# Optimization experiments

Hardware: AMD Instinct MI355X
Metric: run time of the kernel (lower is better)

The kernel has to match this reference:

```python
import jax, jax.numpy as jnp
import numpy as np

C_POW = 8.0  # RGLRU 'c' constant


def setup_inputs() -> dict:
    key = jax.random.key(0)
    ks = jax.random.split(key, 11)
    B, H, K, NB = 4096, 2048, 4, 4
    Hb = H // NB
    s = 1.0 / np.sqrt(H)
    sb = 1.0 / np.sqrt(Hb)
    return {
        "x": jax.random.normal(ks[0], (B, H), jnp.float32),
        "conv_state": jax.random.normal(ks[1], (B, K - 1, H), jnp.float32),
        "rglru_state": jax.random.normal(ks[2], (B, H), jnp.float32),
        "Wg": jax.random.normal(ks[3], (H, H), jnp.float32) * s,
        "Wr": jax.random.normal(ks[4], (H, H), jnp.float32) * s,
        "Wo": jax.random.normal(ks[5], (H, H), jnp.float32) * s,
        "conv_w": jax.random.normal(ks[6], (K, H), jnp.float32) * 0.5,
        "conv_b": jax.random.normal(ks[7], (H,), jnp.float32) * 0.1,
        "Wi": jax.random.normal(ks[8], (NB, Hb, Hb), jnp.float32) * sb,
        "Wrg": jax.random.normal(ks[9], (NB, Hb, Hb), jnp.float32) * sb,
        # a in (0.5, 0.99): valid base for a**(c*r) and sqrt(1 - a^2)
        "a": jax.random.uniform(ks[10], (H,), jnp.float32) * 0.49 + 0.5,
    }


def _block_linear(x, W):
    # x: [B, H], W: [NB, Hb, Hb] block-diagonal linear (torch convention y = x @ W.T per block)
    B = x.shape[0]
    NB, Hb, _ = W.shape
    xb = x.reshape(B, NB, Hb)
    yb = jnp.einsum("bnh,noh->bno", xb, W)
    return yb.reshape(B, NB * Hb)


def reference(x, conv_state, rglru_state, Wg, Wr, Wo, conv_w, conv_b, Wi, Wrg, a):
    # gate branch
    gate = jax.nn.gelu(x @ Wg.T, approximate=False)
    # recurrent branch projection
    xr = x @ Wr.T
    # depthwise causal conv single step: window = [prev K-1 inputs, current]
    window = jnp.concatenate([conv_state, xr[:, None, :]], axis=1)  # [B, K, H]
    xc = jnp.einsum("bkh,kh->bh", window, conv_w) + conv_b
    new_conv_state = window[:, 1:, :]  # [B, K-1, H]
    # RG-LRU single step
    i_t = jax.nn.sigmoid(_block_linear(xc, Wi))
    r_t = jax.nn.sigmoid(_block_linear(xc, Wrg))
    a_t = jnp.power(a, C_POW * r_t)
    multiplier = jnp.sqrt(1.0 - a_t * a_t)
    new_rglru_state = rglru_state * a_t + multiplier * (i_t * xc)
    # output projection of gated state
    out = (gate * new_rglru_state) @ Wo.T
    return out, new_conv_state, new_rglru_state
```

## Files before the change

### kernel.cpp

```cpp
#include <hip/hip_runtime.h>
#include <math.h>

#define BB 4096
#define HH 2048
#define NBK 4
#define HB 512

typedef short bh8 __attribute__((ext_vector_type(8)));
typedef float f32x4 __attribute__((ext_vector_type(4)));

__device__ __forceinline__ float gelu_exact(float v) {
    return 0.5f * v * (1.0f + erff(v * 0.70710678118654752f));
}

__device__ __forceinline__ void cvt_store(char* hiB, char* loB, int row, int cb,
                                          float4 f0, float4 f1) {
    unsigned u0 = __float_as_uint(f0.x), u1 = __float_as_uint(f0.y),
             u2 = __float_as_uint(f0.z), u3 = __float_as_uint(f0.w),
             u4 = __float_as_uint(f1.x), u5 = __float_as_uint(f1.y),
             u6 = __float_as_uint(f1.z), u7 = __float_as_uint(f1.w);
    uint4 H;
    H.x = (u1 & 0xFFFF0000u) | (u0 >> 16);
    H.y = (u3 & 0xFFFF0000u) | (u2 >> 16);
    H.z = (u5 & 0xFFFF0000u) | (u4 >> 16);
    H.w = (u7 & 0xFFFF0000u) | (u6 >> 16);
    float l0 = f0.x - __uint_as_float(u0 & 0xFFFF0000u);
    float l1 = f0.y - __uint_as_float(u1 & 0xFFFF0000u);
    float l2 = f0.z - __uint_as_float(u2 & 0xFFFF0000u);
    float l3 = f0.w - __uint_as_float(u3 & 0xFFFF0000u);
    float l4 = f1.x - __uint_as_float(u4 & 0xFFFF0000u);
    float l5 = f1.y - __uint_as_float(u5 & 0xFFFF0000u);
    float l6 = f1.z - __uint_as_float(u6 & 0xFFFF0000u);
    float l7 = f1.w - __uint_as_float(u7 & 0xFFFF0000u);
    unsigned v0 = __float_as_uint(l0), v1 = __float_as_uint(l1),
             v2 = __float_as_uint(l2), v3 = __float_as_uint(l3),
             v4 = __float_as_uint(l4), v5 = __float_as_uint(l5),
             v6 = __float_as_uint(l6), v7 = __float_as_uint(l7);
    uint4 L;
    L.x = (v1 & 0xFFFF0000u) | (v0 >> 16);
    L.y = (v3 & 0xFFFF0000u) | (v2 >> 16);
    L.z = (v5 & 0xFFFF0000u) | (v4 >> 16);
    L.w = (v7 & 0xFFFF0000u) | (v6 >> 16);
    const int s = (cb ^ ((row >> 1) & 3)) * 16;
    *(uint4*)(hiB + row * 64 + s) = H;
    *(uint4*)(loB + row * 64 + s) = L;
}

template<int EPI>
__global__ __launch_bounds__(256, 2)
void bgemm_bt(const float* __restrict__ A, int lda, long batchA,
              const float* __restrict__ Bm, int ldb, long batchB,
              float* __restrict__ C, int ldc, long batchC, int K)
{
    constexpr int BK = 32;
    __shared__ uint4 ldsv[4096];
    char* lds = (char*)ldsv;

    A  += (long)blockIdx.z * batchA;
    Bm += (long)blockIdx.z * batchB;
    C  += (long)blockIdx.z * batchC;

    const int tid  = threadIdx.x;
    const int row0 = blockIdx.y * 128;
    const int col0 = blockIdx.x * 128;

    const int sr  = tid >> 2;
    const int scb = tid & 3;
    const float* Ald = A  + (long)(row0 + sr) * lda + scb * 8;
    const float* Bld = Bm + (long)(col0 + sr) * ldb + scb * 8;
    const long a64 = 64L * lda, b64 = 64L * ldb;

    const int lane = tid & 63;
    const int wr = (tid >> 7) & 1;
    const int wc = (tid >> 6) & 1;
    const int fm = lane & 15;
    const int kb = lane >> 4;
    const int slot = ((kb ^ ((fm >> 1) & 3)) & 3) * 16;
    const int aoff = (wr * 64 + fm) * 64 + slot;
    const int boff = (wc * 64 + fm) * 64 + slot;

    f32x4 acc[4][4] = {};

    float4 p0, p1, p2, p3, p4, p5, p6, p7;
    p0 = *(const float4*)(Ald);         p1 = *(const float4*)(Ald + 4);
    p2 = *(const float4*)(Ald + a64);   p3 = *(const float4*)(Ald + a64 + 4);
    p4 = *(const float4*)(Bld);         p5 = *(const float4*)(Bld + 4);
    p6 = *(const float4*)(Bld + b64);   p7 = *(const float4*)(Bld + b64 + 4);
    cvt_store(lds,         lds + 8192,  sr,      scb, p0, p1);
    cvt_store(lds,         lds + 8192,  sr + 64, scb, p2, p3);
    cvt_store(lds + 16384, lds + 24576, sr,      scb, p4, p5);
    cvt_store(lds + 16384, lds + 24576, sr + 64, scb, p6, p7);
    __syncthreads();

    const int nkt = K / BK;
    for (int kt = 0; kt < nkt; ++kt) {
        const int cur = (kt & 1) << 15;
        const int nxt = cur ^ 32768;
        if (kt + 1 < nkt) {
            const float* pa = Ald + (kt + 1) * BK;
            const float* pb = Bld + (kt + 1) * BK;
            p0 = *(const float4*)(pa);         p1 = *(const float4*)(pa + 4);
            p2 = *(const float4*)(pa + a64);   p3 = *(const float4*)(pa + a64 + 4);
            p4 = *(const float4*)(pb);         p5 = *(const float4*)(pb + 4);
            p6 = *(const float4*)(pb + b64);   p7 = *(const float4*)(pb + b64 + 4);
        }
        char* Ah = lds + cur;          char* Al = Ah + 8192;
        char* Bh = lds + cur + 16384;  char* Bl = Bh + 8192;
        bh8 ahf[4], alf[4];
        #pragma unroll
        for (int i = 0; i < 4; ++i) {
            ahf[i] = *(const bh8*)(Ah + aoff + i * 1024);
            alf[i] = *(const bh8*)(Al + aoff + i * 1024);
        }
        #pragma unroll
        for (int j = 0; j < 4; ++j) {
            const bh8 bhf = *(const bh8*)(Bh + boff + j * 1024);
            const bh8 blf = *(const bh8*)(Bl + boff + j * 1024);
            #pragma unroll
            for (int i = 0; i < 4; ++i)
                acc[i][j] = __builtin_amdgcn_mfma_f32_16x16x32_bf16(ahf[i], bhf, acc[i][j], 0, 0, 0);
            #pragma unroll
            for (int i = 0; i < 4; ++i)
                acc[i][j] = __builtin_amdgcn_mfma_f32_16x16x32_bf16(ahf[i], blf, acc[i][j], 0, 0, 0);
            #pragma unroll
            for (int i = 0; i < 4; ++i)
                acc[i][j] = __builtin_amdgcn_mfma_f32_16x16x32_bf16(alf[i], bhf, acc[i][j], 0, 0, 0);
        }
        if (kt + 1 < nkt) {
            cvt_store(lds + nxt,         lds + nxt + 8192,  sr,      scb, p0, p1);
            cvt_store(lds + nxt,         lds + nxt + 8192,  sr + 64, scb, p2, p3);
            cvt_store(lds + nxt + 16384, lds + nxt + 24576, sr,      scb, p4, p5);
            cvt_store(lds + nxt + 16384, lds + nxt + 24576, sr + 64, scb, p6, p7);
        }
        __syncthreads();
    }

    const int erow = row0 + wr * 64 + (lane >> 4) * 4;
    const int ecol = col0 + wc * 64 + fm;
    #pragma unroll
    for (int i = 0; i < 4; ++i)
        #pragma unroll
        for (int j = 0; j < 4; ++j)
            #pragma unroll
            for (int r = 0; r < 4; ++r) {
                float v = acc[i][j][r];
                if (EPI == 1) v = gelu_exact(v);
                C[(long)(erow + i * 16 + r) * ldc + ecol + j * 16] = v;
            }
}

__global__ __launch_bounds__(256, 2)
void bd_rglru(const float* __restrict__ xc,
              const float* __restrict__ Wi,
              const float* __restrict__ Wrg,
              const float* __restrict__ rg,
              const float* __restrict__ gate,
              const float* __restrict__ av,
              float* __restrict__ nrs,
              float* __restrict__ hbuf)
{
    constexpr int BK = 32;
    __shared__ uint4 ldsv[3072];
    char* lds = (char*)ldsv;
    char* Ah = lds;          char* Al = lds + 8192;
    char* Ih = lds + 16384;  char* Il = lds + 24576;
    char* Rh = lds + 32768;  char* Rl = lds + 40960;

    const int nb   = blockIdx.z;
    const int tid  = threadIdx.x;
    const int row0 = blockIdx.y * 128;
    const int col0 = blockIdx.x * 128;

    const int sr  = tid >> 2;
    const int scb = tid & 3;
    const float* Ald = xc  + (long)(row0 + sr) * HH + nb * HB + scb * 8;
    const float* Ild = Wi  + (long)nb * HB * HB + (long)(col0 + sr) * HB + scb * 8;
    const float* Rld = Wrg + (long)nb * HB * HB + (long)(col0 + sr) * HB + scb * 8;
    const long a64 = 64L * HH;
    const long w64 = 64L * HB;

    const int lane = tid & 63;
    const int wr = (tid >> 7) & 1;
    const int wc = (tid >> 6) & 1;
    const int fm = lane & 15;
    const int kb = lane >> 4;
    const int slot = ((kb ^ ((fm >> 1) & 3)) & 3) * 16;
    const int aoff = (wr * 64 + fm) * 64 + slot;
    const int boff = (wc * 64 + fm) * 64 + slot;

    f32x4 ai[4][4] = {}, ar[4][4] = {};

    for (int kt = 0; kt < HB / BK; ++kt) {
        const int ko = kt * BK;
        const float4 a0 = *(const float4*)(Ald + ko);
        const float4 a1 = *(const float4*)(Ald + ko + 4);
        const float4 a2 = *(const float4*)(Ald + a64 + ko);
        const float4 a3 = *(const float4*)(Ald + a64 + ko + 4);
        const float4 i0 = *(const float4*)(Ild + ko);
        const float4 i1 = *(const float4*)(Ild + ko + 4);
        const float4 i2 = *(const float4*)(Ild + w64 + ko);
        const float4 i3 = *(const float4*)(Ild + w64 + ko + 4);
        const float4 r0 = *(const float4*)(Rld + ko);
        const float4 r1 = *(const float4*)(Rld + ko + 4);
        const float4 r2 = *(const float4*)(Rld + w64 + ko);
        const float4 r3 = *(const float4*)(Rld + w64 + ko + 4);
        __syncthreads();
        cvt_store(Ah, Al, sr,      scb, a0, a1);
        cvt_store(Ah, Al, sr + 64, scb, a2, a3);
        cvt_store(Ih, Il, sr,      scb, i0, i1);
        cvt_store(Ih, Il, sr + 64, scb, i2, i3);
        cvt_store(Rh, Rl, sr,      scb, r0, r1);
        cvt_store(Rh, Rl, sr + 64, scb, r2, r3);
        __syncthreads();
        bh8 ahf[4], alf[4];
        #pragma unroll
        for (int i = 0; i < 4; ++i) {
            ahf[i] = *(const bh8*)(Ah + aoff + i * 1024);
            alf[i] = *(const bh8*)(Al + aoff + i * 1024);
        }
        #pragma unroll
        for (int j = 0; j < 4; ++j) {
            const bh8 bihf = *(const bh8*)(Ih + boff + j * 1024);
            const bh8 bilf = *(const bh8*)(Il + boff + j * 1024);
            const bh8 brhf = *(const bh8*)(Rh + boff + j * 1024);
            const bh8 brlf = *(const bh8*)(Rl + boff + j * 1024);
            #pragma unroll
            for (int i = 0; i < 4; ++i)
                ai[i][j] = __builtin_amdgcn_mfma_f32_16x16x32_bf16(ahf[i], bihf, ai[i][j], 0, 0, 0);
            #pragma unroll
            for (int i = 0; i < 4; ++i)
                ai[i][j] = __builtin_amdgcn_mfma_f32_16x16x32_bf16(ahf[i], bilf, ai[i][j], 0, 0, 0);
            #pragma unroll
            for (int i = 0; i < 4; ++i)
                ai[i][j] = __builtin_amdgcn_mfma_f32_16x16x32_bf16(alf[i], bihf, ai[i][j], 0, 0, 0);
            #pragma unroll
            for (int i = 0; i < 4; ++i)
                ar[i][j] = __builtin_amdgcn_mfma_f32_16x16x32_bf16(ahf[i], brhf, ar[i][j], 0, 0, 0);
            #pragma unroll
            for (int i = 0; i < 4; ++i)
                ar[i][j] = __builtin_amdgcn_mfma_f32_16x16x32_bf16(ahf[i], brlf, ar[i][j], 0, 0, 0);
            #pragma unroll
            for (int i = 0; i < 4; ++i)
                ar[i][j] = __builtin_amdgcn_mfma_f32_16x16x32_bf16(alf[i], brhf, ar[i][j], 0, 0, 0);
        }
    }

    const int erow = row0 + wr * 64 + (lane >> 4) * 4;
    const int ecolL = col0 + wc * 64 + fm;
    #pragma unroll
    for (int j = 0; j < 4; ++j) {
        const int gcol = nb * HB + ecolL + j * 16;
        const float la8 = 8.0f * logf(av[gcol]);
        #pragma unroll
        for (int i = 0; i < 4; ++i)
            #pragma unroll
            for (int r = 0; r < 4; ++r) {
                const long off = (long)(erow + i * 16 + r) * HH + gcol;
                const float it = 1.0f / (1.0f + expf(-ai[i][j][r]));
                const float rt = 1.0f / (1.0f + expf(-ar[i][j][r]));
                const float at = expf(la8 * rt);
                const float mult = sqrtf(fmaxf(0.0f, 1.0f - at * at));
                const float o = fmaf(rg[off], at, mult * (it * xc[off]));
                nrs[off]  = o;
                hbuf[off] = gate[off] * o;
            }
    }
}

__global__ void conv_kernel(const float* __restrict__ cs,
                            const float* __restrict__ xr,
                            const float* __restrict__ cw,
                            const float* __restrict__ cb,
                            float* __restrict__ xc,
                            float* __restrict__ ncs)
{
    const long idx = (long)blockIdx.x * blockDim.x + threadIdx.x;
    const long n4 = (long)BB * HH / 4;
    if (idx >= n4) return;
    const long b = idx / (HH / 4);
    const int  h = (int)(idx % (HH / 4)) * 4;

    const float4 c0 = *(const float4*)&cs[(b * 3 + 0) * HH + h];
    const float4 c1 = *(const float4*)&cs[(b * 3 + 1) * HH + h];
    const float4 c2 = *(const float4*)&cs[(b * 3 + 2) * HH + h];
    const float4 xv = *(const float4*)&xr[b * HH + h];
    const float4 w0 = *(const float4*)&cw[0 * HH + h];
    const float4 w1 = *(const float4*)&cw[1 * HH + h];
    const float4 w2 = *(const float4*)&cw[2 * HH + h];
    const float4 w3 = *(const float4*)&cw[3 * HH + h];
    const float4 bb = *(const float4*)&cb[h];

    float4 r;
    r.x = fmaf(c0.x, w0.x, fmaf(c1.x, w1.x, fmaf(c2.x, w2.x, fmaf(xv.x, w3.x, bb.x))));
    r.y = fmaf(c0.y, w0.y, fmaf(c1.y, w1.y, fmaf(c2.y, w2.y, fmaf(xv.y, w3.y, bb.y))));
    r.z = fmaf(c0.z, w0.z, fmaf(c1.z, w1.z, fmaf(c2.z, w2.z, fmaf(xv.z, w3.z, bb.z))));
    r.w = fmaf(c0.w, w0.w, fmaf(c1.w, w1.w, fmaf(c2.w, w2.w, fmaf(xv.w, w3.w, bb.w))));

    *(float4*)&xc[b * HH + h] = r;
    *(float4*)&ncs[(b * 3 + 0) * HH + h] = c1;
    *(float4*)&ncs[(b * 3 + 1) * HH + h] = c2;
    *(float4*)&ncs[(b * 3 + 2) * HH + h] = xv;
}

extern "C" void kernel_launch(void* const* d_in, const int* in_sizes, int n_in,
                              void* d_out, int out_size, void* d_ws, size_t ws_size,
                              hipStream_t stream) {
    const float* x    = (const float*)d_in[0];
    const float* cs   = (const float*)d_in[1];
    const float* rg   = (const float*)d_in[2];
    const float* Wg   = (const float*)d_in[3];
    const float* Wr   = (const float*)d_in[4];
    const float* Wo   = (const float*)d_in[5];
    const float* cw   = (const float*)d_in[6];
    const float* cb   = (const float*)d_in[7];
    const float* Wi   = (const float*)d_in[8];
    const float* Wrg  = (const float*)d_in[9];
    const float* av   = (const float*)d_in[10];

    const long BH = (long)BB * HH;
    float* out = (float*)d_out;
    float* ncs = out + BH;
    float* nrs = out + 4 * BH;

    float* ws   = (float*)d_ws;
    float* gate = ws;
    float* xr   = ws + BH;
    float* xc   = ws + 2 * BH;

    const dim3 blk(256);
    const dim3 g1(HH / 128, BB / 128, 1);
    const dim3 g2(HB / 128, BB / 128, NBK);
    const int nElem4 = (int)(BH / 4);
    const dim3 ge((nElem4 + 255) / 256);

    bgemm_bt<1><<<g1, blk, 0, stream>>>(x, HH, 0, Wg, HH, 0, gate, HH, 0, HH);
    bgemm_bt<0><<<g1, blk, 0, stream>>>(x, HH, 0, Wr, HH, 0, xr, HH, 0, HH);
    conv_kernel<<<ge, blk, 0, stream>>>(cs, xr, cw, cb, xc, ncs);
    bd_rglru<<<g2, blk, 0, stream>>>(xc, Wi, Wrg, rg, gate, av, nrs, gate);
    bgemm_bt<0><<<g1, blk, 0, stream>>>(gate, HH, 0, Wo, HH, 0, out, HH, 0, HH);
}
```

Before: 859.0 us.

## Pre-pack weights into split-bf16 tiles and stream them via global_load_lds

```diff
diff --git a/kernel.cpp b/kernel.cpp
--- a/kernel.cpp
+++ b/kernel.cpp
@@ -8,18 +8,18 @@
 
 typedef short bh8 __attribute__((ext_vector_type(8)));
 typedef float f32x4 __attribute__((ext_vector_type(4)));
+typedef unsigned int u32;
 
 __device__ __forceinline__ float gelu_exact(float v) {
     return 0.5f * v * (1.0f + erff(v * 0.70710678118654752f));
 }
 
-__device__ __forceinline__ void cvt_store(char* hiB, char* loB, int row, int cb,
-                                          float4 f0, float4 f1) {
-    unsigned u0 = __float_as_uint(f0.x), u1 = __float_as_uint(f0.y),
-             u2 = __float_as_uint(f0.z), u3 = __float_as_uint(f0.w),
-             u4 = __float_as_uint(f1.x), u5 = __float_as_uint(f1.y),
-             u6 = __float_as_uint(f1.z), u7 = __float_as_uint(f1.w);
-    uint4 H;
+__device__ __forceinline__ void cvt8(const float4 f0, const float4 f1,
+                                     uint4& H, uint4& L) {
+    u32 u0 = __float_as_uint(f0.x), u1 = __float_as_uint(f0.y),
+        u2 = __float_as_uint(f0.z), u3 = __float_as_uint(f0.w),
+        u4 = __float_as_uint(f1.x), u5 = __float_as_uint(f1.y),
+        u6 = __float_as_uint(f1.z), u7 = __float_as_uint(f1.w);
     H.x = (u1 & 0xFFFF0000u) | (u0 >> 16);
     H.y = (u3 & 0xFFFF0000u) | (u2 >> 16);
     H.z = (u5 & 0xFFFF0000u) | (u4 >> 16);
@@ -32,33 +32,60 @@
     float l5 = f1.y - __uint_as_float(u5 & 0xFFFF0000u);
     float l6 = f1.z - __uint_as_float(u6 & 0xFFFF0000u);
     float l7 = f1.w - __uint_as_float(u7 & 0xFFFF0000u);
-    unsigned v0 = __float_as_uint(l0), v1 = __float_as_uint(l1),
-             v2 = __float_as_uint(l2), v3 = __float_as_uint(l3),
-             v4 = __float_as_uint(l4), v5 = __float_as_uint(l5),
-             v6 = __float_as_uint(l6), v7 = __float_as_uint(l7);
-    uint4 L;
+    u32 v0 = __float_as_uint(l0), v1 = __float_as_uint(l1),
+        v2 = __float_as_uint(l2), v3 = __float_as_uint(l3),
+        v4 = __float_as_uint(l4), v5 = __float_as_uint(l5),
+        v6 = __float_as_uint(l6), v7 = __float_as_uint(l7);
     L.x = (v1 & 0xFFFF0000u) | (v0 >> 16);
     L.y = (v3 & 0xFFFF0000u) | (v2 >> 16);
     L.z = (v5 & 0xFFFF0000u) | (v4 >> 16);
     L.w = (v7 & 0xFFFF0000u) | (v6 >> 16);
+}
+
+__device__ __forceinline__ void cvt_store(char* hiB, char* loB, int row, int cb,
+                                          float4 f0, float4 f1) {
+    uint4 H, L;
+    cvt8(f0, f1, H, L);
     const int s = (cb ^ ((row >> 1) & 3)) * 16;
     *(uint4*)(hiB + row * 64 + s) = H;
     *(uint4*)(loB + row * 64 + s) = L;
 }
 
+__device__ __forceinline__ void gload_lds16(const u32* g, char* l) {
+    __builtin_amdgcn_global_load_lds(
+        (const __attribute__((address_space(1))) u32*)g,
+        (__attribute__((address_space(3))) u32*)l, 16, 0, 0);
+}
+
+__global__ void pack_w(const float* __restrict__ W, u32* __restrict__ P,
+                       int N, int K, int rowShift)
+{
+    const int idx = blockIdx.x * 256 + threadIdx.x;
+    if (idx >= (N << rowShift)) return;
+    const int n   = idx >> rowShift;
+    const int rem = idx & ((1 << rowShift) - 1);
+    const int t   = rem >> 2;
+    const int g   = rem & 3;
+    const float* src = W + (long)n * K + t * 32 + g * 8;
+    uint4 H, L;
+    cvt8(*(const float4*)src, *(const float4*)(src + 4), H, L);
+    u32* blk = P + ((long)n * (K >> 5) + t) * 32;
+    *(uint4*)(blk + g * 4)      = H;
+    *(uint4*)(blk + 16 + g * 4) = L;
+}
+
 template<int EPI>
 __global__ __launch_bounds__(256, 2)
-void bgemm_bt(const float* __restrict__ A, int lda, long batchA,
-              const float* __restrict__ Bm, int ldb, long batchB,
-              float* __restrict__ C, int ldc, long batchC, int K)
+void bgemm_pw(const float* __restrict__ A,
+              const u32* __restrict__ Bp,
+              float* __restrict__ C)
 {
-    constexpr int BK = 32;
-    __shared__ uint4 ldsv[4096];
+    __shared__ uint4 ldsv[3072];
     char* lds = (char*)ldsv;
-
-    A  += (long)blockIdx.z * batchA;
-    Bm += (long)blockIdx.z * batchB;
-    C  += (long)blockIdx.z * batchC;
+    char* Ah = lds;
+    char* Al = lds + 8192;
+    char* B0 = lds + 16384;
+    char* B1 = lds + 32768;
 
     const int tid  = threadIdx.x;
     const int row0 = blockIdx.y * 128;
@@ -66,46 +93,55 @@
 
     const int sr  = tid >> 2;
     const int scb = tid & 3;
-    const float* Ald = A  + (long)(row0 + sr) * lda + scb * 8;
-    const float* Bld = Bm + (long)(col0 + sr) * ldb + scb * 8;
-    const long a64 = 64L * lda, b64 = 64L * ldb;
+    const float* Ald = A + (long)(row0 + sr) * HH + scb * 8;
+    const long a64 = 64L * HH;
 
     const int lane = tid & 63;
+    const int w    = tid >> 6;
     const int wr = (tid >> 7) & 1;
     const int wc = (tid >> 6) & 1;
     const int fm = lane & 15;
     const int kb = lane >> 4;
-    const int slot = ((kb ^ ((fm >> 1) & 3)) & 3) * 16;
-    const int aoff = (wr * 64 + fm) * 64 + slot;
-    const int boff = (wc * 64 + fm) * 64 + slot;
+    const int fr7 = fm & 7;
+
+    const int aslot = ((kb ^ ((fm >> 1) & 3)) & 3) * 16;
+    const int aoff  = (wr * 64 + fm) * 64 + aslot;
+    const int bbase  = (wc * 64 + fm) * 128;
+    const int bhioff = bbase + ((kb ^ fr7) * 16);
+    const int blooff = bbase + (((4 | kb) ^ fr7) * 16);
+
+    const int lrow8 = lane >> 3;
+    const int slog  = (lane & 7) ^ lrow8;
+    const int rloc  = w * 32;
+    const u32* bsrc[4];
+    #pragma unroll
+    for (int i = 0; i < 4; ++i)
+        bsrc[i] = Bp + ((long)(col0 + rloc + i * 8 + lrow8) * (HH / 32)) * 32 + slog * 4;
 
     f32x4 acc[4][4] = {};
 
-    float4 p0, p1, p2, p3, p4, p5, p6, p7;
-    p0 = *(const float4*)(Ald);         p1 = *(const float4*)(Ald + 4);
-    p2 = *(const float4*)(Ald + a64);   p3 = *(const float4*)(Ald + a64 + 4);
-    p4 = *(const float4*)(Bld);         p5 = *(const float4*)(Bld + 4);
-    p6 = *(const float4*)(Bld + b64);   p7 = *(const float4*)(Bld + b64 + 4);
-    cvt_store(lds,         lds + 8192,  sr,      scb, p0, p1);
-    cvt_store(lds,         lds + 8192,  sr + 64, scb, p2, p3);
-    cvt_store(lds + 16384, lds + 24576, sr,      scb, p4, p5);
-    cvt_store(lds + 16384, lds + 24576, sr + 64, scb, p6, p7);
-    __syncthreads();
-
-    const int nkt = K / BK;
+    float4 p0 = *(const float4*)(Ald),       p1 = *(const float4*)(Ald + 4);
+    float4 p2 = *(const float4*)(Ald + a64), p3 = *(const float4*)(Ald + a64 + 4);
+    #pragma unroll
+    for (int i = 0; i < 4; ++i)
+        gload_lds16(bsrc[i], B0 + (rloc + i * 8) * 128);
+
+    const int nkt = HH / 32;
     for (int kt = 0; kt < nkt; ++kt) {
-        const int cur = (kt & 1) << 15;
-        const int nxt = cur ^ 32768;
+        __syncthreads();
+        cvt_store(Ah, Al, sr,      scb, p0, p1);
+        cvt_store(Ah, Al, sr + 64, scb, p2, p3);
+        __syncthreads();
         if (kt + 1 < nkt) {
-            const float* pa = Ald + (kt + 1) * BK;
-            const float* pb = Bld + (kt + 1) * BK;
-            p0 = *(const float4*)(pa);         p1 = *(const float4*)(pa + 4);
-            p2 = *(const float4*)(pa + a64);   p3 = *(const float4*)(pa + a64 + 4);
-            p4 = *(const float4*)(pb);         p5 = *(const float4*)(pb + 4);
-            p6 = *(const float4*)(pb + b64);   p7 = *(const float4*)(pb + b64 + 4);
-        }
-        char* Ah = lds + cur;          char* Al = Ah + 8192;
-        char* Bh = lds + cur + 16384;  char* Bl = Bh + 8192;
+            const float* pa = Ald + (kt + 1) * 32;
+            p0 = *(const float4*)(pa);        p1 = *(const float4*)(pa + 4);
+            p2 = *(const float4*)(pa + a64);  p3 = *(const float4*)(pa + a64 + 4);
+            char* Bn = (kt & 1) ? B0 : B1;
+            #pragma unroll
+            for (int i = 0; i < 4; ++i)
+                gload_lds16(bsrc[i] + (kt + 1) * 32, Bn + (rloc + i * 8) * 128);
+        }
+        const char* Bc = (kt & 1) ? B1 : B0;
         bh8 ahf[4], alf[4];
         #pragma unroll
         for (int i = 0; i < 4; ++i) {
@@ -114,8 +150,8 @@
         }
         #pragma unroll
         for (int j = 0; j < 4; ++j) {
-            const bh8 bhf = *(const bh8*)(Bh + boff + j * 1024);
-            const bh8 blf = *(const bh8*)(Bl + boff + j * 1024);
+            const bh8 bhf = *(const bh8*)(Bc + bhioff + j * 2048);
+            const bh8 blf = *(const bh8*)(Bc + blooff + j * 2048);
             #pragma unroll
             for (int i = 0; i < 4; ++i)
                 acc[i][j] = __builtin_amdgcn_mfma_f32_16x16x32_bf16(ahf[i], bhf, acc[i][j], 0, 0, 0);
@@ -126,13 +162,6 @@
             for (int i = 0; i < 4; ++i)
                 acc[i][j] = __builtin_amdgcn_mfma_f32_16x16x32_bf16(alf[i], bhf, acc[i][j], 0, 0, 0);
         }
-        if (kt + 1 < nkt) {
-            cvt_store(lds + nxt,         lds + nxt + 8192,  sr,      scb, p0, p1);
-            cvt_store(lds + nxt,         lds + nxt + 8192,  sr + 64, scb, p2, p3);
-            cvt_store(lds + nxt + 16384, lds + nxt + 24576, sr,      scb, p4, p5);
-            cvt_store(lds + nxt + 16384, lds + nxt + 24576, sr + 64, scb, p6, p7);
-        }
-        __syncthreads();
     }
 
     const int erow = row0 + wr * 64 + (lane >> 4) * 4;
@@ -145,26 +174,25 @@
             for (int r = 0; r < 4; ++r) {
                 float v = acc[i][j][r];
                 if (EPI == 1) v = gelu_exact(v);
-                C[(long)(erow + i * 16 + r) * ldc + ecol + j * 16] = v;
+                C[(long)(erow + i * 16 + r) * HH + ecol + j * 16] = v;
             }
 }
 
 __global__ __launch_bounds__(256, 2)
 void bd_rglru(const float* __restrict__ xc,
-              const float* __restrict__ Wi,
-              const float* __restrict__ Wrg,
+              const u32* __restrict__ Wip,
+              const u32* __restrict__ Wrp,
               const float* __restrict__ rg,
-              const float* __restrict__ gate,
+              const float* gate,
               const float* __restrict__ av,
               float* __restrict__ nrs,
-              float* __restrict__ hbuf)
+              float* hbuf)
 {
-    constexpr int BK = 32;
-    __shared__ uint4 ldsv[3072];
+    __shared__ uint4 ldsv[5120];
     char* lds = (char*)ldsv;
-    char* Ah = lds;          char* Al = lds + 8192;
-    char* Ih = lds + 16384;  char* Il = lds + 24576;
-    char* Rh = lds + 32768;  char* Rl = lds + 40960;
+    char* Ah = lds;            char* Al = lds + 8192;
+    char* I0 = lds + 16384;    char* I1 = lds + 32768;
+    char* R0 = lds + 49152;    char* R1 = lds + 65536;
 
     const int nb   = blockIdx.z;
     const int tid  = threadIdx.x;
@@ -173,45 +201,65 @@
 
     const int sr  = tid >> 2;
     const int scb = tid & 3;
-    const float* Ald = xc  + (long)(row0 + sr) * HH + nb * HB + scb * 8;
-    const float* Ild = Wi  + (long)nb * HB * HB + (long)(col0 + sr) * HB + scb * 8;
-    const float* Rld = Wrg + (long)nb * HB * HB + (long)(col0 + sr) * HB + scb * 8;
+    const float* Ald = xc + (long)(row0 + sr) * HH + nb * HB + scb * 8;
     const long a64 = 64L * HH;
-    const long w64 = 64L * HB;
 
     const int lane = tid & 63;
+    const int w    = tid >> 6;
     const int wr = (tid >> 7) & 1;
     const int wc = (tid >> 6) & 1;
     const int fm = lane & 15;
     const int kb = lane >> 4;
-    const int slot = ((kb ^ ((fm >> 1) & 3)) & 3) * 16;
-    const int aoff = (wr * 64 + fm) * 64 + slot;
-    const int boff = (wc * 64 + fm) * 64 + slot;
+    const int fr7 = fm & 7;
+
+    const int aslot = ((kb ^ ((fm >> 1) & 3)) & 3) * 16;
+    const int aoff  = (wr * 64 + fm) * 64 + aslot;
+    const int bbase  = (wc * 64 + fm) * 128;
+    const int bhioff = bbase + ((kb ^ fr7) * 16);
+    const int blooff = bbase + (((4 | kb) ^ fr7) * 16);
+
+    const int lrow8 = lane >> 3;
+    const int slog  = (lane & 7) ^ lrow8;
+    const int rloc  = w * 32;
+    const u32* isrc[4];
+    const u32* rsrc[4];
+    #pragma unroll
+    for (int i = 0; i < 4; ++i) {
+        const long nrow = (long)(nb * HB + col0 + rloc + i * 8 + lrow8) * (HB / 32);
+        isrc[i] = Wip + nrow * 32 + slog * 4;
+        rsrc[i] = Wrp + nrow * 32 + slog * 4;
+    }
 
     f32x4 ai[4][4] = {}, ar[4][4] = {};
 
-    for (int kt = 0; kt < HB / BK; ++kt) {
-        const int ko = kt * BK;
-        const float4 a0 = *(const float4*)(Ald + ko);
-        const float4 a1 = *(const float4*)(Ald + ko + 4);
-        const float4 a2 = *(const float4*)(Ald + a64 + ko);
-        const float4 a3 = *(const float4*)(Ald + a64 + ko + 4);
-        const float4 i0 = *(const float4*)(Ild + ko);
-        const float4 i1 = *(const float4*)(Ild + ko + 4);
-        const float4 i2 = *(const float4*)(Ild + w64 + ko);
-        const float4 i3 = *(const float4*)(Ild + w64 + ko + 4);
-        const float4 r0 = *(const float4*)(Rld + ko);
-        const float4 r1 = *(const float4*)(Rld + ko + 4);
-        const float4 r2 = *(const float4*)(Rld + w64 + ko);
-        const float4 r3 = *(const float4*)(Rld + w64 + ko + 4);
+    float4 p0 = *(const float4*)(Ald),       p1 = *(const float4*)(Ald + 4);
+    float4 p2 = *(const float4*)(Ald + a64), p3 = *(const float4*)(Ald + a64 + 4);
+    #pragma unroll
+    for (int i = 0; i < 4; ++i) {
+        gload_lds16(isrc[i], I0 + (rloc + i * 8) * 128);
+        gload_lds16(rsrc[i], R0 + (rloc + i * 8) * 128);
+    }
+
+    const int nkt = HB / 32;
+    for (int kt = 0; kt < nkt; ++kt) {
         __syncthreads();
-        cvt_store(Ah, Al, sr,      scb, a0, a1);
-        cvt_store(Ah, Al, sr + 64, scb, a2, a3);
-        cvt_store(Ih, Il, sr,      scb, i0, i1);
-        cvt_store(Ih, Il, sr + 64, scb, i2, i3);
-        cvt_store(Rh, Rl, sr,      scb, r0, r1);
-        cvt_store(Rh, Rl, sr + 64, scb, r2, r3);
+        cvt_store(Ah, Al, sr,      scb, p0, p1);
+        cvt_store(Ah, Al, sr + 64, scb, p2, p3);
         __syncthreads();
+        if (kt + 1 < nkt) {
+            const float* pa = Ald + (kt + 1) * 32;
+            p0 = *(const float4*)(pa);        p1 = *(const float4*)(pa + 4);
+            p2 = *(const float4*)(pa + a64);  p3 = *(const float4*)(pa + a64 + 4);
+            char* In = (kt & 1) ? I0 : I1;
+            char* Rn = (kt & 1) ? R0 : R1;
+            #pragma unroll
+            for (int i = 0; i < 4; ++i) {
+                gload_lds16(isrc[i] + (kt + 1) * 32, In + (rloc + i * 8) * 128);
+                gload_lds16(rsrc[i] + (kt + 1) * 32, Rn + (rloc + i * 8) * 128);
+            }
+        }
+        const char* Ic = (kt & 1) ? I1 : I0;
+        const char* Rc = (kt & 1) ? R1 : R0;
         bh8 ahf[4], alf[4];
         #pragma unroll
         for (int i = 0; i < 4; ++i) {
@@ -220,10 +268,10 @@
         }
         #pragma unroll
         for (int j = 0; j < 4; ++j) {
-            const bh8 bihf = *(const bh8*)(Ih + boff + j * 1024);
-            const bh8 bilf = *(const bh8*)(Il + boff + j * 1024);
-            const bh8 brhf = *(const bh8*)(Rh + boff + j * 1024);
-            const bh8 brlf = *(const bh8*)(Rl + boff + j * 1024);
+            const bh8 bihf = *(const bh8*)(Ic + bhioff + j * 2048);
+            const bh8 bilf = *(const bh8*)(Ic + blooff + j * 2048);
+            const bh8 brhf = *(const bh8*)(Rc + bhioff + j * 2048);
+            const bh8 brlf = *(const bh8*)(Rc + blooff + j * 2048);
             #pragma unroll
             for (int i = 0; i < 4; ++i)
                 ai[i][j] = __builtin_amdgcn_mfma_f32_16x16x32_bf16(ahf[i], bihf, ai[i][j], 0, 0, 0);
@@ -268,10 +316,9 @@
 }
 
 __global__ void conv_kernel(const float* __restrict__ cs,
-                            const float* __restrict__ xr,
                             const float* __restrict__ cw,
                             const float* __restrict__ cb,
-                            float* __restrict__ xc,
+                            float* xcio,
                             float* __restrict__ ncs)
 {
     const long idx = (long)blockIdx.x * blockDim.x + threadIdx.x;
@@ -283,7 +330,7 @@
     const float4 c0 = *(const float4*)&cs[(b * 3 + 0) * HH + h];
     const float4 c1 = *(const float4*)&cs[(b * 3 + 1) * HH + h];
     const float4 c2 = *(const float4*)&cs[(b * 3 + 2) * HH + h];
-    const float4 xv = *(const float4*)&xr[b * HH + h];
+    const float4 xv = *(const float4*)&xcio[b * HH + h];
     const float4 w0 = *(const float4*)&cw[0 * HH + h];
     const float4 w1 = *(const float4*)&cw[1 * HH + h];
     const float4 w2 = *(const float4*)&cw[2 * HH + h];
@@ -296,7 +343,7 @@
     r.z = fmaf(c0.z, w0.z, fmaf(c1.z, w1.z, fmaf(c2.z, w2.z, fmaf(xv.z, w3.z, bb.z))));
     r.w = fmaf(c0.w, w0.w, fmaf(c1.w, w1.w, fmaf(c2.w, w2.w, fmaf(xv.w, w3.w, bb.w))));
 
-    *(float4*)&xc[b * HH + h] = r;
+    *(float4*)&xcio[b * HH + h] = r;
     *(float4*)&ncs[(b * 3 + 0) * HH + h] = c1;
     *(float4*)&ncs[(b * 3 + 1) * HH + h] = c2;
     *(float4*)&ncs[(b * 3 + 2) * HH + h] = xv;
@@ -324,18 +371,26 @@
 
     float* ws   = (float*)d_ws;
     float* gate = ws;
-    float* xr   = ws + BH;
-    float* xc   = ws + 2 * BH;
+    float* xcio = ws + BH;
+    u32*   wpk  = (u32*)(ws + 2 * BH);
+    u32*   wip  = wpk;
+    u32*   wrp  = wpk + (long)NBK * HB * HB;
 
     const dim3 blk(256);
     const dim3 g1(HH / 128, BB / 128, 1);
     const dim3 g2(HB / 128, BB / 128, NBK);
-    const int nElem4 = (int)(BH / 4);
-    const dim3 ge((nElem4 + 255) / 256);
-
-    bgemm_bt<1><<<g1, blk, 0, stream>>>(x, HH, 0, Wg, HH, 0, gate, HH, 0, HH);
-    bgemm_bt<0><<<g1, blk, 0, stream>>>(x, HH, 0, Wr, HH, 0, xr, HH, 0, HH);
-    conv_kernel<<<ge, blk, 0, stream>>>(cs, xr, cw, cb, xc, ncs);
-    bd_rglru<<<g2, blk, 0, stream>>>(xc, Wi, Wrg, rg, gate, av, nrs, gate);
-    bgemm_bt<0><<<g1, blk, 0, stream>>>(gate, HH, 0, Wo, HH, 0, out, HH, 0, HH);
-}
+    const dim3 ge((int)(BH / 4 / 256));
+    const int pdense = (HH * (HH / 8) + 255) / 256;
+    const int pbd    = (NBK * HB * (HB / 8) + 255) / 256;
+
+    pack_w<<<pdense, blk, 0, stream>>>(Wg, wpk, HH, HH, 8);
+    bgemm_pw<1><<<g1, blk, 0, stream>>>(x, wpk, gate);
+    pack_w<<<pdense, blk, 0, stream>>>(Wr, wpk, HH, HH, 8);
+    bgemm_pw<0><<<g1, blk, 0, stream>>>(x, wpk, xcio);
+    conv_kernel<<<ge, blk, 0, stream>>>(cs, cw, cb, xcio, ncs);
+    pack_w<<<pbd, blk, 0, stream>>>(Wi,  wip, NBK * HB, HB, 6);
+    pack_w<<<pbd, blk, 0, stream>>>(Wrg, wrp, NBK * HB, HB, 6);
+    bd_rglru<<<g2, blk, 0, stream>>>(xcio, wip, wrp, rg, gate, av, nrs, gate);
+    pack_w<<<pdense, blk, 0, stream>>>(Wo, wpk, HH, HH, 8);
+    bgemm_pw<0><<<g1, blk, 0, stream>>>(gate, wpk, out);
+}
```

After: 861.4 us. Within noise of the previous version (+0.3%).
